# Performance work log

Hardware: AMD Instinct MI355X
Metric: run time of the kernel (lower is better)

## Reference

```python
import jax, jax.numpy as jnp
import numpy as np
from jax import lax

B, CIN, H, W = 16, 64, 128, 128
NUM_CLASSES = 80
K = 100              # cfg.TEST.TOPK
SCORE_THRESH = 0.2   # hardcoded in decode()
NMS_THRESH = 0.5     # cfg.TEST.NMS_THRESH
RATIO = 4.0          # inp_downsample_ratio


def setup_inputs() -> dict:
    key = jax.random.key(0)
    ks = jax.random.split(key, 8)
    def w(k, shape, scale=0.05):
        return jax.random.normal(k, shape, dtype=jnp.float32) * scale
    inp = {"x": jax.random.normal(ks[0], (B, CIN, H, W), dtype=jnp.float32)}
    for i, (name, cout) in enumerate([("cls", NUM_CLASSES), ("reg", 2), ("wh", 2)]):
        inp[f"{name}_w1"] = w(ks[1 + 2 * i], (64, CIN, 3, 3))
        inp[f"{name}_b1"] = jnp.zeros((64,), jnp.float32)
        inp[f"{name}_w2"] = w(ks[2 + 2 * i], (cout, 64, 1, 1))
        # cls 1x1 conv bias filled with -2.19 as in the torch module
        inp[f"{name}_b2"] = jnp.full((cout,), -2.19 if name == "cls" else 0.0, jnp.float32)
    return inp


def _conv(x, w, b):
    y = lax.conv_general_dilated(x, w, (1, 1), 'SAME',
                                 dimension_numbers=('NCHW', 'OIHW', 'NCHW'))
    return y + b[None, :, None, None]


def _branch(x, w1, b1, w2, b2):
    return _conv(jax.nn.relu(_conv(x, w1, b1)), w2, b2)


def _nms_keep(boxes, valid):
    # boxes: [K,4] sorted by score desc (top_k output); valid: [K] bool
    x1, y1, x2, y2 = boxes[:, 0], boxes[:, 1], boxes[:, 2], boxes[:, 3]
    area = (x2 - x1) * (y2 - y1)
    iw = jnp.clip(jnp.minimum(x2[:, None], x2[None, :]) - jnp.maximum(x1[:, None], x1[None, :]), 0.0)
    ih = jnp.clip(jnp.minimum(y2[:, None], y2[None, :]) - jnp.maximum(y1[:, None], y1[None, :]), 0.0)
    inter = iw * ih
    iou = inter / (area[:, None] + area[None, :] - inter + 1e-9)  # [K,K]
    idx = jnp.arange(K)
    def step(keep, i):
        sup = (iou[i] > NMS_THRESH) & (idx > i) & keep[i]
        return keep & ~sup, None
    keep, _ = lax.scan(step, valid, idx)
    return keep


def reference(x, cls_w1, cls_b1, cls_w2, cls_b2,
              reg_w1, reg_b1, reg_w2, reg_b2,
              wh_w1, wh_b1, wh_w2, wh_b2):
    cls = jax.nn.sigmoid(_branch(x, cls_w1, cls_b1, cls_w2, cls_b2))  # [B,C,H,W]
    reg = jax.nn.sigmoid(_branch(x, reg_w1, reg_b1, reg_w2, reg_b2))  # [B,2,H,W]
    wh = jnp.exp(_branch(x, wh_w1, wh_b1, wh_w2, wh_b2))              # [B,2,H,W]

    # 3x3 max-pool peak NMS (torch max_pool2d pads with -inf; SAME matches k=3,s=1,p=1)
    pooled = lax.reduce_window(cls, -jnp.inf, lax.max, (1, 1, 3, 3), (1, 1, 1, 1), 'SAME')
    cls = cls * (pooled == cls).astype(cls.dtype)

    cls_f = cls.transpose(0, 2, 3, 1).reshape(B, H * W, NUM_CLASSES)
    reg_f = reg.transpose(0, 2, 3, 1).reshape(B, H * W, 2)
    wh_f = wh.transpose(0, 2, 3, 1).reshape(B, H * W, 2)

    scores_all = jnp.max(cls_f, axis=-1)              # [B,HW]
    cats_all = jnp.argmax(cls_f, axis=-1)             # [B,HW]
    scores, inds = lax.top_k(scores_all, K)           # [B,K], sorted desc
    valid = scores > SCORE_THRESH                     # fixed-size mask instead of dynamic filter

    cats = jnp.take_along_axis(cats_all, inds, axis=1)
    reg_k = jnp.take_along_axis(reg_f, inds[..., None], axis=1)   # [B,K,2]
    wh_k = jnp.take_along_axis(wh_f, inds[..., None], axis=1)     # [B,K,2]

    gy, gx = jnp.meshgrid(jnp.arange(H), jnp.arange(W), indexing='ij')
    grids = jnp.stack([gx, gy], axis=-1).reshape(-1, 2).astype(jnp.float32)  # [HW,2] (x,y)
    ct = grids[inds] + reg_k                                       # [B,K,2]
    boxes = jnp.concatenate([ct - wh_k / 2.0, ct + wh_k / 2.0], axis=-1) * RATIO  # [B,K,4]

    keep = jax.vmap(_nms_keep)(boxes, valid)          # [B,K] bool
    return boxes, cats, scores, keep
```

## Files before the change

### kernel.cpp

```cpp
#include <hip/hip_runtime.h>
#include <math.h>

#define BN 16
#define HWSZ 16384
#define NC 80
#define KK 100

typedef _Float16 f16;
typedef _Float16 f16x2 __attribute__((ext_vector_type(2)));
typedef _Float16 f16x4 __attribute__((ext_vector_type(4)));
typedef _Float16 f16x8 __attribute__((ext_vector_type(8)));
typedef float    f32x4 __attribute__((ext_vector_type(4)));
typedef unsigned int uint;
typedef unsigned long long u64;

#define WS_CLS   0
#define CLS_SZ   (BN*NC*HWSZ)
#define WS_REG   (WS_CLS + CLS_SZ)
#define REG_SZ   (BN*2*HWSZ)
#define WS_WH    (WS_REG + REG_SZ)
#define WH_SZ    (BN*2*HWSZ)
#define WS_SC    (WS_WH + WH_SZ)
#define SC_SZ    (BN*HWSZ)
#define WS_CAT   (WS_SC + SC_SZ)
#define CAT_SZ   (BN*HWSZ)
#define WS_W1H   (WS_CAT + CAT_SZ)
#define W1F      (110592/2)
#define WS_W1L   (WS_W1H + W1F)
#define WS_W2H   (WS_W1L + W1F)
#define W2F      (7168/2)
#define WS_W2L   (WS_W2H + W2F)
#define NREG     (BN*128*2*2)
#define WS_XTH   (WS_W2L + W2F)
#define XT_F     (NREG*2112/2)
#define WS_XTL   (WS_XTH + XT_F)
#define WS_ZR    (WS_XTL + XT_F)
#define ZR_F     1056
#define WS_SC1   (WS_ZR + ZR_F)
#define WS_CAT1  (WS_SC1 + SC_SZ)
#define WS_END2  (WS_CAT1 + CAT_SZ)

#define SCL_X   16.0f
#define SCL_W   256.0f
#define INV_ACC (1.0f/4096.0f)

#define GL2LDS(g, l) __builtin_amdgcn_global_load_lds( \
    (__attribute__((address_space(1))) unsigned int*)(unsigned long long)(const void*)(g), \
    (__attribute__((address_space(3))) unsigned int*)(unsigned int)(unsigned long long)(void*)(l), \
    16, 0, 0)

__global__ void k_prep(const float* __restrict__ cw1, const float* __restrict__ rw1,
                       const float* __restrict__ ww1, const float* __restrict__ cw2,
                       const float* __restrict__ rw2, const float* __restrict__ ww2,
                       f16* __restrict__ w1h, f16* __restrict__ w1l,
                       f16* __restrict__ w2h, f16* __restrict__ w2l,
                       float* __restrict__ zr) {
    int idx = blockIdx.x * 256 + threadIdx.x;
    if (idx < 3*9*64*64) {
        int ci = idx & 63, co = (idx >> 6) & 63;
        int s  = (idx >> 12) % 9, br = idx / 36864;
        const float* src = (br == 0) ? cw1 : (br == 1 ? rw1 : ww1);
        float v = src[(co*64 + ci)*9 + s] * SCL_W;
        f16 h = (f16)v;
        w1h[idx] = h; w1l[idx] = (f16)(v - (float)h);
    }
    int j = idx - 3*9*64*64;
    if (j >= 0 && j < 112*64) {
        int ci = j & 63, row = j >> 6;
        float v = 0.f;
        if (row < 80)                    v = cw2[row*64 + ci];
        else if (row < 82)               v = rw2[(row-80)*64 + ci];
        else if (row >= 96 && row < 98)  v = ww2[(row-96)*64 + ci];
        v *= SCL_W;
        f16 h = (f16)v;
        w2h[j] = h; w2l[j] = (f16)(v - (float)h);
    }
    if (zr && idx < ZR_F) zr[idx] = 0.f;
}

__global__ __launch_bounds__(256) void k_prepx(const float* __restrict__ x,
                                               f16* __restrict__ xth,
                                               f16* __restrict__ xtl) {
    const int reg = blockIdx.x;
    const int chunk = reg & 1, hh = (reg >> 1) & 1;
    const int gy = (reg >> 2) & 127, b = reg >> 9;
    __shared__ f16 th[66*72] __attribute__((aligned(16)));
    __shared__ f16 tl[66*72] __attribute__((aligned(16)));
    const int tid = threadIdx.x;
    const float* xb = x + ((size_t)(b*64 + chunk*32))*HWSZ + gy*128;
    #pragma unroll
    for (int it = 0; it < 9; it++) {
        int idx = it*256 + tid;
        if (idx < 2112) {
            int ci = idx / 66, pxi = idx - ci*66;
            int gp = hh*64 - 1 + pxi;
            float v = 0.f;
            if (gp >= 0 && gp < 128) v = xb[(size_t)ci*HWSZ + gp] * SCL_X;
            f16 hv = (f16)v;
            th[pxi*72 + ci] = hv;
            tl[pxi*72 + ci] = (f16)(v - (float)hv);
        }
    }
    __syncthreads();
    f16* oh = xth + (size_t)reg*2112;
    f16* ol = xtl + (size_t)reg*2112;
    {
        int row = tid >> 2, q = tid & 3;
        int sq = q ^ ((row >> 1) & 3);
        *(f16x8*)(oh + row*32 + sq*8) = *(const f16x8*)(th + row*72 + q*8);
        *(f16x8*)(ol + row*32 + sq*8) = *(const f16x8*)(tl + row*72 + q*8);
        if (tid < 8) {
            int u2 = 256 + tid, row2 = u2 >> 2, q2 = u2 & 3;
            int sq2 = q2 ^ ((row2 >> 1) & 3);
            *(f16x8*)(oh + row2*32 + sq2*8) = *(const f16x8*)(th + row2*72 + q2*8);
            *(f16x8*)(ol + row2*32 + sq2*8) = *(const f16x8*)(tl + row2*72 + q2*8);
        }
    }
}

#define ABUF 8448
__global__ __launch_bounds__(256) void k_conv(
    const f16* __restrict__ xth, const f16* __restrict__ xtl, const f16* __restrict__ zreg,
    const f16* __restrict__ w1h, const f16* __restrict__ w1l,
    const f16* __restrict__ w2h, const f16* __restrict__ w2l,
    const float* __restrict__ b1c, const float* __restrict__ b1r, const float* __restrict__ b1w,
    const float* __restrict__ b2c, const float* __restrict__ b2r, const float* __restrict__ b2w,
    float* __restrict__ cls_o, float* __restrict__ reg_o, float* __restrict__ wh_o)
{
    __shared__ char smem[6*ABUF] __attribute__((aligned(16)));
    f16* Rh = (f16*)smem;
    f16* Rl = (f16*)(smem + 9216);

    const int p  = blockIdx.x + 2*blockIdx.y + 256*blockIdx.z;
    const int lg = (p & 7)*512 + (p >> 3);
    const int b  = lg >> 8;
    const int y  = (lg & 255) >> 1;
    const int h  = lg & 1;

    const int tid = threadIdx.x;
    const int w = tid >> 6, lane = tid & 63;
    const int l15 = lane & 15, quad = lane >> 4;

    static const int CS[6] = {0,0,0,1,1,1};
    static const int RS[6] = {0,1,2,0,1,2};

    #pragma unroll
    for (int si = 0; si < 6; si++) {
        const int gy_ = y - 1 + RS[si];
        const f16* sh_; const f16* sl_;
        if (gy_ >= 0 && gy_ < 128) {
            size_t ro_ = (size_t)(((b*128 + gy_)*2 + h)*2 + CS[si]) * 2112;
            sh_ = xth + ro_; sl_ = xtl + ro_;
        } else { sh_ = zreg; sl_ = zreg; }
        char* db_ = smem + si*ABUF;
        GL2LDS(sh_ + tid*8, db_ + tid*16);
        GL2LDS(sl_ + tid*8, db_ + 4224 + tid*16);
        if (tid < 8) {
            GL2LDS(sh_ + 2048 + tid*8, db_ + 4096 + tid*16);
            GL2LDS(sl_ + 2048 + tid*8, db_ + 4224 + 4096 + tid*16);
        }
    }

    f32x4 acc[3][4];
    #pragma unroll
    for (int br = 0; br < 3; br++)
        #pragma unroll
        for (int m = 0; m < 4; m++) acc[br][m] = (f32x4){0.f,0.f,0.f,0.f};

    __syncthreads();

    for (int si = 0; si < 6; si++) {
        const f16* APh = (const f16*)(smem + si*ABUF);
        const f16* APl = APh + 2112;
        const int chunk = CS[si], r = RS[si];
        #pragma unroll
        for (int dx = 0; dx < 3; dx++) {
            const int s = r*3 + dx;
            f16x8 bh[3], bl[3];
            #pragma unroll
            for (int br = 0; br < 3; br++) {
                size_t k = ((size_t)((br*9 + s)*64 + (w*16 + l15)))*64 + chunk*32 + quad*8;
                bh[br] = *(const f16x8*)(w1h + k);
                bl[br] = *(const f16x8*)(w1l + k);
            }
            #pragma unroll
            for (int m = 0; m < 4; m++) {
                const int row = m*16 + l15 + dx;
                const int off = row*32 + ((quad ^ ((row >> 1) & 3)) << 3);
                f16x8 ah = *(const f16x8*)(APh + off);
                f16x8 al = *(const f16x8*)(APl + off);
                #pragma unroll
                for (int br = 0; br < 3; br++) {
                    acc[br][m] = __builtin_amdgcn_mfma_f32_16x16x32_f16(ah, bh[br], acc[br][m], 0,0,0);
                    acc[br][m] = __builtin_amdgcn_mfma_f32_16x16x32_f16(ah, bl[br], acc[br][m], 0,0,0);
                    acc[br][m] = __builtin_amdgcn_mfma_f32_16x16x32_f16(al, bh[br], acc[br][m], 0,0,0);
                }
            }
        }
    }

    #pragma unroll
    for (int br = 0; br < 3; br++) {
        const float* b1 = (br == 0) ? b1c : (br == 1 ? b1r : b1w);
        const float b1v = b1[w*16 + l15];
        __syncthreads();
        #pragma unroll
        for (int m = 0; m < 4; m++)
            #pragma unroll
            for (int rg = 0; rg < 4; rg++) {
                float t = fmaxf(acc[br][m][rg]*INV_ACC + b1v, 0.f) * SCL_X;
                f16 hh = (f16)t;
                int pxl = m*16 + quad*4 + rg;
                int co  = w*16 + l15;
                Rh[pxl*72 + co] = hh;
                Rl[pxl*72 + co] = (f16)(t - (float)hh);
            }
        __syncthreads();

        const int NT     = (br == 0) ? 5 : 1;
        const int rowoff = (br == 0) ? 0 : (br == 1 ? 80 : 96);
        f32x4 a2[5];
        #pragma unroll
        for (int n = 0; n < 5; n++) a2[n] = (f32x4){0.f,0.f,0.f,0.f};

        #pragma unroll
        for (int kc = 0; kc < 64; kc += 32) {
            int off = (w*16 + l15)*72 + kc + quad*8;
            f16x8 xh = *(const f16x8*)(Rh + off);
            f16x8 xl = *(const f16x8*)(Rl + off);
            #pragma unroll
            for (int n = 0; n < 5; n++) {
                if (n >= NT) break;
                const f16* g2h = w2h + (rowoff + n*16 + l15)*64 + kc + quad*8;
                const f16* g2l = w2l + (rowoff + n*16 + l15)*64 + kc + quad*8;
                f16x8 bh = *(const f16x8*)g2h;
                f16x8 bl = *(const f16x8*)g2l;
                a2[n] = __builtin_amdgcn_mfma_f32_16x16x32_f16(xh, bh, a2[n], 0,0,0);
                a2[n] = __builtin_amdgcn_mfma_f32_16x16x32_f16(xh, bl, a2[n], 0,0,0);
                a2[n] = __builtin_amdgcn_mfma_f32_16x16x32_f16(xl, bh, a2[n], 0,0,0);
            }
        }

        const int pxg = h*64 + w*16 + quad*4;
        if (br == 0) {
            #pragma unroll
            for (int n = 0; n < 5; n++) {
                int co2 = n*16 + l15;
                float bb = b2c[co2];
                #pragma unroll
                for (int rg = 0; rg < 4; rg++) {
                    float sv = a2[n][rg]*INV_ACC + bb;
                    cls_o[((size_t)(b*80 + co2)*128 + y)*128 + pxg + rg] = 1.f/(1.f + expf(-sv));
                }
            }
        } else {
            if (l15 < 2) {
                const float* b2 = (br == 1) ? b2r : b2w;
                float* outp     = (br == 1) ? reg_o : wh_o;
                float bb = b2[l15];
                #pragma unroll
                for (int rg = 0; rg < 4; rg++) {
                    float sv = a2[0][rg]*INV_ACC + bb;
                    float o  = (br == 1) ? (1.f/(1.f + expf(-sv))) : expf(sv);
                    outp[((size_t)(b*2 + l15))*HWSZ + y*128 + pxg + rg] = o;
                }
            }
        }
    }
}

#define A_STRIDE 36
#define ABUF_FB  9504
__global__ __launch_bounds__(256) void k_conv_fb(
    const float* __restrict__ x,
    const f16* __restrict__ w1h, const f16* __restrict__ w1l,
    const f16* __restrict__ w2h, const f16* __restrict__ w2l,
    const float* __restrict__ b1c, const float* __restrict__ b1r, const float* __restrict__ b1w,
    const float* __restrict__ b2c, const float* __restrict__ b2r, const float* __restrict__ b2w,
    float* __restrict__ cls_o, float* __restrict__ reg_o, float* __restrict__ wh_o)
{
    __shared__ char smem[19008] __attribute__((aligned(16)));
    f16* Rh = (f16*)smem;
    f16* Rl = (f16*)(smem + 9216);

    const int h = blockIdx.x, y = blockIdx.y, b = blockIdx.z;
    const int tid = threadIdx.x;
    const int w = tid >> 6, lane = tid & 63;
    const int l15 = lane & 15, quad = lane >> 4;

    static const int CS[6] = {0,0,0,1,1,1};
    static const int RS[6] = {0,1,2,0,1,2};

    #define STAGEF(bufi, si_) do {                                            \
        const int gy = y - 1 + RS[si_];                                       \
        const bool ok = (gy >= 0) && (gy < 128);                              \
        const float* xp = x + ((size_t)(b*64 + CS[si_]*32)*128 + gy)*128;     \
        f16x2* dh = (f16x2*)(smem + (bufi)*ABUF_FB);                          \
        f16x2* dl = (f16x2*)(smem + (bufi)*ABUF_FB + 4752);                   \
        _Pragma("unroll")                                                     \
        for (int e0 = 0; e0 < 1024; e0 += 256) {                              \
            int e = e0 + tid;                                                 \
            int pxl = e & 63, cp = e >> 6;                                    \
            float v0 = 0.f, v1 = 0.f;                                         \
            if (ok) { int g = h*64 + pxl;                                     \
                      v0 = xp[(size_t)(2*cp)*HWSZ + g]*SCL_X;                 \
                      v1 = xp[(size_t)(2*cp+1)*HWSZ + g]*SCL_X; }             \
            f16 h0 = (f16)v0, h1 = (f16)v1;                                   \
            f16 l0 = (f16)(v0 - (float)h0), l1 = (f16)(v1 - (float)h1);       \
            int wi = (pxl + 1)*18 + cp;                                       \
            dh[wi] = (f16x2){h0, h1};                                         \
            dl[wi] = (f16x2){l0, l1};                                         \
        }                                                                     \
        if (tid < 32) {                                                       \
            int side = tid >> 4, cp = tid & 15;                               \
            bool valid = ok && (side ? (h == 0) : (h == 1));                  \
            int g = side ? 64 : 63;                                           \
            float v0 = 0.f, v1 = 0.f;                                         \
            if (valid) { v0 = xp[(size_t)(2*cp)*HWSZ + g]*SCL_X;              \
                         v1 = xp[(size_t)(2*cp+1)*HWSZ + g]*SCL_X; }          \
            f16 h0 = (f16)v0, h1 = (f16)v1;                                   \
            f16 l0 = (f16)(v0 - (float)h0), l1 = (f16)(v1 - (float)h1);       \
            int wi = (side ? 65 : 0)*18 + cp;                                 \
            dh[wi] = (f16x2){h0, h1};                                         \
            dl[wi] = (f16x2){l0, l1};                                         \
        }                                                                     \
    } while (0)

    f32x4 acc[3][4];
    #pragma unroll
    for (int br = 0; br < 3; br++)
        #pragma unroll
        for (int m = 0; m < 4; m++) acc[br][m] = (f32x4){0.f,0.f,0.f,0.f};

    STAGEF(0, 0);
    __syncthreads();

    for (int si = 0; si < 6; si++) {
        const int cur = si & 1;
        if (si < 5) STAGEF(cur ^ 1, si + 1);
        const f16* APh = (const f16*)(smem + cur*ABUF_FB);
        const f16* APl = APh + 2376;
        const int chunk = CS[si], r = RS[si];
        #pragma unroll
        for (int dx = 0; dx < 3; dx++) {
            const int s = r*3 + dx;
            f16x8 bh[3], bl[3];
            #pragma unroll
            for (int br = 0; br < 3; br++) {
                size_t k = ((size_t)((br*9 + s)*64 + (w*16 + l15)))*64 + chunk*32 + quad*8;
                bh[br] = *(const f16x8*)(w1h + k);
                bl[br] = *(const f16x8*)(w1l + k);
            }
            #pragma unroll
            for (int m = 0; m < 4; m++) {
                int off = (m*16 + l15 + dx)*A_STRIDE + quad*8;
                f16x4 h0 = *(const f16x4*)(APh + off);
                f16x4 h1 = *(const f16x4*)(APh + off + 4);
                f16x4 u0 = *(const f16x4*)(APl + off);
                f16x4 u1 = *(const f16x4*)(APl + off + 4);
                f16x8 ah = __builtin_shufflevector(h0, h1, 0,1,2,3,4,5,6,7);
                f16x8 al = __builtin_shufflevector(u0, u1, 0,1,2,3,4,5,6,7);
                #pragma unroll
                for (int br = 0; br < 3; br++) {
                    acc[br][m] = __builtin_amdgcn_mfma_f32_16x16x32_f16(ah, bh[br], acc[br][m], 0,0,0);
                    acc[br][m] = __builtin_amdgcn_mfma_f32_16x16x32_f16(ah, bl[br], acc[br][m], 0,0,0);
                    acc[br][m] = __builtin_amdgcn_mfma_f32_16x16x32_f16(al, bh[br], acc[br][m], 0,0,0);
                }
            }
        }
        __syncthreads();
    }
    #undef STAGEF

    #pragma unroll
    for (int br = 0; br < 3; br++) {
        const float* b1 = (br == 0) ? b1c : (br == 1 ? b1r : b1w);
        const float b1v = b1[w*16 + l15];
        __syncthreads();
        #pragma unroll
        for (int m = 0; m < 4; m++)
            #pragma unroll
            for (int rg = 0; rg < 4; rg++) {
                float t = fmaxf(acc[br][m][rg]*INV_ACC + b1v, 0.f) * SCL_X;
                f16 hh = (f16)t;
                int pxl = m*16 + quad*4 + rg;
                int co  = w*16 + l15;
                Rh[pxl*72 + co] = hh;
                Rl[pxl*72 + co] = (f16)(t - (float)hh);
            }
        __syncthreads();

        const int NT     = (br == 0) ? 5 : 1;
        const int rowoff = (br == 0) ? 0 : (br == 1 ? 80 : 96);
        f32x4 a2[5];
        #pragma unroll
        for (int n = 0; n < 5; n++) a2[n] = (f32x4){0.f,0.f,0.f,0.f};

        #pragma unroll
        for (int kc = 0; kc < 64; kc += 32) {
            int off = (w*16 + l15)*72 + kc + quad*8;
            f16x8 xh = *(const f16x8*)(Rh + off);
            f16x8 xl = *(const f16x8*)(Rl + off);
            #pragma unroll
            for (int n = 0; n < 5; n++) {
                if (n >= NT) break;
                const f16* g2h = w2h + (rowoff + n*16 + l15)*64 + kc + quad*8;
                const f16* g2l = w2l + (rowoff + n*16 + l15)*64 + kc + quad*8;
                f16x8 bh = *(const f16x8*)g2h;
                f16x8 bl = *(const f16x8*)g2l;
                a2[n] = __builtin_amdgcn_mfma_f32_16x16x32_f16(xh, bh, a2[n], 0,0,0);
                a2[n] = __builtin_amdgcn_mfma_f32_16x16x32_f16(xh, bl, a2[n], 0,0,0);
                a2[n] = __builtin_amdgcn_mfma_f32_16x16x32_f16(xl, bh, a2[n], 0,0,0);
            }
        }

        const int pxg = h*64 + w*16 + quad*4;
        if (br == 0) {
            #pragma unroll
            for (int n = 0; n < 5; n++) {
                int co2 = n*16 + l15;
                float bb = b2c[co2];
                #pragma unroll
                for (int rg = 0; rg < 4; rg++) {
                    float sv = a2[n][rg]*INV_ACC + bb;
                    cls_o[((size_t)(b*80 + co2)*128 + y)*128 + pxg + rg] = 1.f/(1.f + expf(-sv));
                }
            }
        } else {
            if (l15 < 2) {
                const float* b2 = (br == 1) ? b2r : b2w;
                float* outp     = (br == 1) ? reg_o : wh_o;
                float bb = b2[l15];
                #pragma unroll
                for (int rg = 0; rg < 4; rg++) {
                    float sv = a2[0][rg]*INV_ACC + bb;
                    float o  = (br == 1) ? (1.f/(1.f + expf(-sv))) : expf(sv);
                    outp[((size_t)(b*2 + l15))*HWSZ + y*128 + pxg + rg] = o;
                }
            }
        }
    }
}

__global__ __launch_bounds__(256) void k_peaks(const float* __restrict__ cls,
                                               float* __restrict__ scA,
                                               int* __restrict__ catA,
                                               float* __restrict__ scB,
                                               int* __restrict__ catB,
                                               int span) {
    const int b  = blockIdx.y;
    const int z  = blockIdx.z;
    const int c0 = z * span, c1 = c0 + span;
    float* __restrict__ sc  = z ? scB  : scA;
    int*   __restrict__ cat = z ? catB : catA;
    const int wv = threadIdx.x >> 6;
    const int l  = threadIdx.x & 63;
    const int y  = blockIdx.x * 4 + wv;
    const int p0 = l * 2;
    const bool yt = (y > 0), yb = (y < 127);
    float best0 = -1.f, best1 = -1.f;
    int bc0 = c0, bc1 = c0;
    for (int c = c0; c < c1; c++) {
        const float* pl = cls + (size_t)(b*80 + c)*HWSZ + y*128 + p0;
        float2 cur = *(const float2*)pl;
        float2 tp  = yt ? *(const float2*)(pl - 128) : make_float2(-1e30f, -1e30f);
        float2 bt  = yb ? *(const float2*)(pl + 128) : make_float2(-1e30f, -1e30f);
        float vm0 = fmaxf(cur.x, fmaxf(tp.x, bt.x));
        float vm1 = fmaxf(cur.y, fmaxf(tp.y, bt.y));
        float lft = __shfl_up(vm1, 1);   if (l == 0)  lft = -1e30f;
        float rgt = __shfl_down(vm0, 1); if (l == 63) rgt = -1e30f;
        float m0 = fmaxf(lft, fmaxf(vm0, vm1));
        float m1 = fmaxf(vm0, fmaxf(vm1, rgt));
        float k0 = (cur.x == m0) ? cur.x : 0.f;
        float k1 = (cur.y == m1) ? cur.y : 0.f;
        if (k0 > best0) { best0 = k0; bc0 = c; }
        if (k1 > best1) { best1 = k1; bc1 = c; }
    }
    int o = b*HWSZ + y*128 + p0;
    *(float2*)&sc[o] = make_float2(best0, best1);
    *(int2*)&cat[o]  = make_int2(bc0, bc1);
}

__global__ __launch_bounds__(256) void k_merge(float* __restrict__ sc0,
                                               int* __restrict__ cat0,
                                               const float* __restrict__ sc1,
                                               const int* __restrict__ cat1) {
    int i = (blockIdx.x * 256 + threadIdx.x) * 4;
    float4 a = *(const float4*)(sc0 + i);
    float4 bq = *(const float4*)(sc1 + i);
    int4   ca = *(const int4*)(cat0 + i);
    int4   cb = *(const int4*)(cat1 + i);
    if (bq.x > a.x) { a.x = bq.x; ca.x = cb.x; }
    if (bq.y > a.y) { a.y = bq.y; ca.y = cb.y; }
    if (bq.z > a.z) { a.z = bq.z; ca.z = cb.z; }
    if (bq.w > a.w) { a.w = bq.w; ca.w = cb.w; }
    *(float4*)(sc0 + i) = a;
    *(int4*)(cat0 + i)  = ca;
}

__global__ __launch_bounds__(256) void k_select(const float* __restrict__ sc,
                                                const int* __restrict__ cats,
                                                const float* __restrict__ regp,
                                                const float* __restrict__ whp,
                                                float* __restrict__ out) {
    const int b   = blockIdx.x;
    const int tid = threadIdx.x;
    const int wv  = tid >> 6, lane = tid & 63;
    const float* scb = sc + (size_t)b*HWSZ;

    __shared__ int   red[2][4];
    __shared__ uint  wtot[4];
    __shared__ int   gib[128];
    __shared__ uint  gvb[128];
    __shared__ int   ebuf[KK];
    __shared__ u64   keys[128];
    __shared__ int   s_inds[KK];
    __shared__ float s_vals[KK];
    __shared__ float X1[KK], Y1[KK], X2[KK], Y2[KK], AR[KK];

    f32x4 d[16];
    #pragma unroll
    for (int c = 0; c < 16; c++)
        d[c] = *(const f32x4*)(scb + c*1024 + tid*4);

    #define CNT_GT(T, OUTV) do {                                              \
        int myc_ = 0;                                                         \
        _Pragma("unroll")                                                     \
        for (int c = 0; c < 16; c++) {                                        \
            _Pragma("unroll")                                                 \
            for (int j = 0; j < 4; j++)                                       \
                myc_ += (__float_as_uint(d[c][j]) > (T)) ? 1 : 0;             \
        }                                                                     \
        _Pragma("unroll")                                                     \
        for (int o_ = 32; o_ >= 1; o_ >>= 1) myc_ += __shfl_xor(myc_, o_);    \
        if (lane == 0) red[par][wv] = myc_;                                   \
        __syncthreads();                                                      \
        OUTV = red[par][0] + red[par][1] + red[par][2] + red[par][3];         \
        par ^= 1;                                                             \
    } while (0)

    int par = 0;
    uint Vbits; uint G;
    {
        int tot0; CNT_GT(0u, tot0);
        if (tot0 < KK) { Vbits = 0u; G = (uint)tot0; }
        else {
            uint lo = 0u, hi = 0x7F800000u; int gHi = 0;
            while (hi - lo > 1u) {
                uint mid = lo + ((hi - lo) >> 1);
                int t_; CNT_GT(mid, t_);
                if (t_ >= KK) lo = mid; else { hi = mid; gHi = t_; }
            }
            Vbits = hi; G = (uint)gHi;
        }
    }
    #undef CNT_GT
    const uint Eneed = KK - G;

    f32x4 c4[16];
    #pragma unroll
    for (int c = 0; c < 16; c++)
        c4[c] = *(const f32x4*)(scb + tid*64 + c*4);

    uint cntG = 0, cntE = 0;
    #pragma unroll
    for (int c = 0; c < 16; c++)
        #pragma unroll
        for (int j = 0; j < 4; j++) {
            uint u = __float_as_uint(c4[c][j]);
            cntG += (u > Vbits) ? 1u : 0u;
            cntE += (u == Vbits) ? 1u : 0u;
        }
    uint pk = (cntE << 16) | cntG;
    uint v = pk;
    #pragma unroll
    for (int o = 1; o <= 32; o <<= 1) {
        uint ov = __shfl_up(v, o);
        if (lane >= o) v += ov;
    }
    if (lane == 63) wtot[wv] = v;
    __syncthreads();
    uint woff = 0;
    for (int i = 0; i < 4; i++) if (i < wv) woff += wtot[i];
    uint excl = v - pk + woff;
    uint pG = excl & 0xFFFFu, pE = excl >> 16;

    #pragma unroll
    for (int c = 0; c < 16; c++)
        #pragma unroll
        for (int j = 0; j < 4; j++) {
            uint u = __float_as_uint(c4[c][j]);
            int idx = tid*64 + c*4 + j;
            if (u > Vbits) { gib[pG] = idx; gvb[pG] = u; pG++; }
            else if (u == Vbits) { if (pE < Eneed) ebuf[pE] = idx; pE++; }
        }
    __syncthreads();

    if (tid < 128)
        keys[tid] = (tid < (int)G) ? (((u64)(~gvb[tid]) << 32) | (uint)gib[tid])
                                   : ~0ull;
    for (uint k2 = 2; k2 <= 128; k2 <<= 1) {
        for (uint j = k2 >> 1; j > 0; j >>= 1) {
            __syncthreads();
            if (tid < 128) {
                uint i = (uint)tid, ixj = i ^ j;
                if (ixj > i) {
                    u64 a = keys[i], bb = keys[ixj];
                    bool up = ((i & k2) == 0);
                    if ((a > bb) == up) { keys[i] = bb; keys[ixj] = a; }
                }
            }
        }
    }
    __syncthreads();

    if (tid < KK) {
        if (tid < (int)G) {
            u64 kk2 = keys[tid];
            s_inds[tid] = (int)(uint)kk2;
            s_vals[tid] = __uint_as_float(~(uint)(kk2 >> 32));
        } else {
            s_inds[tid] = ebuf[tid - (int)G];
            s_vals[tid] = __uint_as_float(Vbits);
        }
    }
    __syncthreads();

    if (tid < KK) {
        int ind   = s_inds[tid];
        float scv = s_vals[tid];
        const float* rb = regp + (size_t)b*2*HWSZ;
        const float* wb = whp  + (size_t)b*2*HWSZ;
        float r0 = rb[ind], r1 = rb[HWSZ + ind];
        float w0 = wb[ind], w1 = wb[HWSZ + ind];
        float ctx = (float)(ind & 127) + r0;
        float cty = (float)(ind >> 7) + r1;
        float x1 = (ctx - w0*0.5f)*4.f, y1 = (cty - w1*0.5f)*4.f;
        float x2 = (ctx + w0*0.5f)*4.f, y2 = (cty + w1*0.5f)*4.f;
        size_t bo = ((size_t)b*KK + tid)*4;
        out[bo+0] = x1; out[bo+1] = y1; out[bo+2] = x2; out[bo+3] = y2;
        out[BN*KK*4 + b*KK + tid]         = (float)cats[(size_t)b*HWSZ + ind];
        out[BN*KK*4 + BN*KK + b*KK + tid] = scv;
        X1[tid] = x1; Y1[tid] = y1; X2[tid] = x2; Y2[tid] = y2;
        AR[tid] = (x2 - x1)*(y2 - y1);
    }
    __syncthreads();

    if (tid < 64) {
        const int l = tid;
        float x1a = X1[l], y1a = Y1[l], x2a = X2[l], y2a = Y2[l], ara = AR[l];
        int   ka  = (s_vals[l] > 0.2f) ? 1 : 0;
        float x1b = 0, y1b = 0, x2b = 0, y2b = 0, arb = 0;
        int   kb  = 0;
        if (l < KK - 64) {
            x1b = X1[64+l]; y1b = Y1[64+l]; x2b = X2[64+l]; y2b = Y2[64+l];
            arb = AR[64+l];
            kb  = (s_vals[64+l] > 0.2f) ? 1 : 0;
        }
        for (int i = 0; i < KK; i++) {
            float jx1, jy1, jx2, jy2, jar; int jk;
            if (i < 64) {
                jx1 = __shfl(x1a, i); jy1 = __shfl(y1a, i);
                jx2 = __shfl(x2a, i); jy2 = __shfl(y2a, i);
                jar = __shfl(ara, i); jk  = __shfl(ka,  i);
            } else {
                int li = i - 64;
                jx1 = __shfl(x1b, li); jy1 = __shfl(y1b, li);
                jx2 = __shfl(x2b, li); jy2 = __shfl(y2b, li);
                jar = __shfl(arb, li); jk  = __shfl(kb,  li);
            }
            if (jk) {
                if (ka && l > i) {
                    float iw = fminf(jx2, x2a) - fmaxf(jx1, x1a); iw = iw > 0.f ? iw : 0.f;
                    float ih = fminf(jy2, y2a) - fmaxf(jy1, y1a); ih = ih > 0.f ? ih : 0.f;
                    float inter = iw*ih;
                    float iou = inter / (jar + ara - inter + 1e-9f);
                    if (iou > 0.5f) ka = 0;
                }
                if (kb && (64 + l) > i) {
                    float iw = fminf(jx2, x2b) - fmaxf(jx1, x1b); iw = iw > 0.f ? iw : 0.f;
                    float ih = fminf(jy2, y2b) - fmaxf(jy1, y1b); ih = ih > 0.f ? ih : 0.f;
                    float inter = iw*ih;
                    float iou = inter / (jar + arb - inter + 1e-9f);
                    if (iou > 0.5f) kb = 0;
                }
            }
        }
        int koff = BN*KK*4 + 2*BN*KK;
        out[koff + b*KK + l] = ka ? 1.f : 0.f;
        if (l < KK - 64) out[koff + b*KK + 64 + l] = kb ? 1.f : 0.f;
    }
}

extern "C" void kernel_launch(void* const* d_in, const int* in_sizes, int n_in,
                              void* d_out, int out_size, void* d_ws, size_t ws_size,
                              hipStream_t stream) {
    const float* x      = (const float*)d_in[0];
    const float* cls_w1 = (const float*)d_in[1];
    const float* cls_b1 = (const float*)d_in[2];
    const float* cls_w2 = (const float*)d_in[3];
    const float* cls_b2 = (const float*)d_in[4];
    const float* reg_w1 = (const float*)d_in[5];
    const float* reg_b1 = (const float*)d_in[6];
    const float* reg_w2 = (const float*)d_in[7];
    const float* reg_b2 = (const float*)d_in[8];
    const float* wh_w1  = (const float*)d_in[9];
    const float* wh_b1  = (const float*)d_in[10];
    const float* wh_w2  = (const float*)d_in[11];
    const float* wh_b2  = (const float*)d_in[12];

    float* ws   = (float*)d_ws;
    float* clsb = ws + WS_CLS;
    float* regb = ws + WS_REG;
    float* whb  = ws + WS_WH;
    float* scw  = ws + WS_SC;
    int*   cat  = (int*)(ws + WS_CAT);
    f16*   w1h  = (f16*)(ws + WS_W1H);
    f16*   w1l  = (f16*)(ws + WS_W1L);
    f16*   w2h  = (f16*)(ws + WS_W2H);
    f16*   w2l  = (f16*)(ws + WS_W2L);
    f16*   xth  = (f16*)(ws + WS_XTH);
    f16*   xtl  = (f16*)(ws + WS_XTL);
    f16*   zr   = (f16*)(ws + WS_ZR);
    float* sc1  = ws + WS_SC1;
    int*   cat1 = (int*)(ws + WS_CAT1);
    float* out  = (float*)d_out;

    const bool big = ws_size >= (size_t)WS_END2 * 4u;

    k_prep<<<(3*9*64*64 + 112*64 + 255)/256, 256, 0, stream>>>(
        cls_w1, reg_w1, wh_w1, cls_w2, reg_w2, wh_w2, w1h, w1l, w2h, w2l,
        big ? (float*)(ws + WS_ZR) : (float*)0);
    if (big) {
        k_prepx<<<NREG, 256, 0, stream>>>(x, xth, xtl);
        k_conv<<<dim3(2, 128, 16), 256, 0, stream>>>(
            xth, xtl, zr, w1h, w1l, w2h, w2l, cls_b1, reg_b1, wh_b1,
            cls_b2, reg_b2, wh_b2, clsb, regb, whb);
        k_peaks<<<dim3(32, 16, 2), 256, 0, stream>>>(clsb, scw, cat, sc1, cat1, 40);
        k_merge<<<256, 256, 0, stream>>>(scw, cat, sc1, cat1);
    } else {
        k_conv_fb<<<dim3(2, 128, 16), 256, 0, stream>>>(
            x, w1h, w1l, w2h, w2l, cls_b1, reg_b1, wh_b1,
            cls_b2, reg_b2, wh_b2, clsb, regb, whb);
        k_peaks<<<dim3(32, 16, 1), 256, 0, stream>>>(clsb, scw, cat, scw, cat, 80);
    }
    k_select<<<16, 256, 0, stream>>>(scw, cat, regb, whb, out);
}
```

Baseline: 490.1 us.

## Compute two output rows per conv block and split peak search four ways

The 3x3 conv kernel now produces two adjacent output rows per block. It stages four input rows per channel chunk and reuses each weight fragment for two accumulator sets, which cuts the grid in half and lowers redundant input and weight loads. LDS drops from six row buffers to four, and launch bounds request two blocks per CU, but doubling the accumulators raises register pressure. Separately, the peak search is split across four class slices instead of two, with a four-way merge kernel, at the cost of a larger workspace requirement.

```diff
diff --git a/kernel.cpp b/kernel.cpp
--- a/kernel.cpp
+++ b/kernel.cpp
@@ -38,7 +38,11 @@
 #define ZR_F     1056
 #define WS_SC1   (WS_ZR + ZR_F)
 #define WS_CAT1  (WS_SC1 + SC_SZ)
-#define WS_END2  (WS_CAT1 + CAT_SZ)
+#define WS_SC2   (WS_CAT1 + CAT_SZ)
+#define WS_CAT2  (WS_SC2 + SC_SZ)
+#define WS_SC3   (WS_CAT2 + CAT_SZ)
+#define WS_CAT3  (WS_SC3 + SC_SZ)
+#define WS_END4  (WS_CAT3 + CAT_SZ)
 
 #define SCL_X   16.0f
 #define SCL_W   256.0f
@@ -119,7 +123,7 @@
 }
 
 #define ABUF 8448
-__global__ __launch_bounds__(256) void k_conv(
+__global__ __launch_bounds__(256, 2) void k_conv(
     const f16* __restrict__ xth, const f16* __restrict__ xtl, const f16* __restrict__ zreg,
     const f16* __restrict__ w1h, const f16* __restrict__ w1l,
     const f16* __restrict__ w2h, const f16* __restrict__ w2l,
@@ -127,146 +131,166 @@
     const float* __restrict__ b2c, const float* __restrict__ b2r, const float* __restrict__ b2w,
     float* __restrict__ cls_o, float* __restrict__ reg_o, float* __restrict__ wh_o)
 {
-    __shared__ char smem[6*ABUF] __attribute__((aligned(16)));
+    __shared__ char smem[4*ABUF] __attribute__((aligned(16)));
     f16* Rh = (f16*)smem;
     f16* Rl = (f16*)(smem + 9216);
 
-    const int p  = blockIdx.x + 2*blockIdx.y + 256*blockIdx.z;
-    const int lg = (p & 7)*512 + (p >> 3);
-    const int b  = lg >> 8;
-    const int y  = (lg & 255) >> 1;
+    const int p  = blockIdx.x + 2*blockIdx.y + 128*blockIdx.z;
+    const int lg = (p & 7)*256 + (p >> 3);
+    const int b  = lg >> 7;
+    const int y0 = ((lg & 127) >> 1) * 2;
     const int h  = lg & 1;
 
     const int tid = threadIdx.x;
     const int w = tid >> 6, lane = tid & 63;
     const int l15 = lane & 15, quad = lane >> 4;
-
-    static const int CS[6] = {0,0,0,1,1,1};
-    static const int RS[6] = {0,1,2,0,1,2};
-
-    #pragma unroll
-    for (int si = 0; si < 6; si++) {
-        const int gy_ = y - 1 + RS[si];
-        const f16* sh_; const f16* sl_;
-        if (gy_ >= 0 && gy_ < 128) {
-            size_t ro_ = (size_t)(((b*128 + gy_)*2 + h)*2 + CS[si]) * 2112;
-            sh_ = xth + ro_; sl_ = xtl + ro_;
-        } else { sh_ = zreg; sl_ = zreg; }
-        char* db_ = smem + si*ABUF;
-        GL2LDS(sh_ + tid*8, db_ + tid*16);
-        GL2LDS(sl_ + tid*8, db_ + 4224 + tid*16);
-        if (tid < 8) {
-            GL2LDS(sh_ + 2048 + tid*8, db_ + 4096 + tid*16);
-            GL2LDS(sl_ + 2048 + tid*8, db_ + 4224 + 4096 + tid*16);
-        }
-    }
-
-    f32x4 acc[3][4];
+    const int co = w*16 + l15;
+
+    #define STAGE4(ch) do {                                                   \
+        _Pragma("unroll")                                                     \
+        for (int gyi = 0; gyi < 4; gyi++) {                                   \
+            const int gy_ = y0 - 1 + gyi;                                     \
+            const f16* sh_; const f16* sl_;                                   \
+            if (gy_ >= 0 && gy_ < 128) {                                      \
+                size_t ro_ = (size_t)(((b*128 + gy_)*2 + h)*2 + (ch)) * 2112; \
+                sh_ = xth + ro_; sl_ = xtl + ro_;                             \
+            } else { sh_ = zreg; sl_ = zreg; }                                \
+            char* db_ = smem + gyi*ABUF;                                      \
+            GL2LDS(sh_ + tid*8, db_ + tid*16);                                \
+            GL2LDS(sl_ + tid*8, db_ + 4224 + tid*16);                         \
+            if (tid < 8) {                                                    \
+                GL2LDS(sh_ + 2048 + tid*8, db_ + 4096 + tid*16);              \
+                GL2LDS(sl_ + 2048 + tid*8, db_ + 4224 + 4096 + tid*16);       \
+            }                                                                 \
+        }                                                                     \
+    } while (0)
+
+    f32x4 accA[3][4], accB[3][4];
     #pragma unroll
     for (int br = 0; br < 3; br++)
         #pragma unroll
-        for (int m = 0; m < 4; m++) acc[br][m] = (f32x4){0.f,0.f,0.f,0.f};
-
-    __syncthreads();
-
-    for (int si = 0; si < 6; si++) {
-        const f16* APh = (const f16*)(smem + si*ABUF);
-        const f16* APl = APh + 2112;
-        const int chunk = CS[si], r = RS[si];
-        #pragma unroll
-        for (int dx = 0; dx < 3; dx++) {
-            const int s = r*3 + dx;
-            f16x8 bh[3], bl[3];
-            #pragma unroll
-            for (int br = 0; br < 3; br++) {
-                size_t k = ((size_t)((br*9 + s)*64 + (w*16 + l15)))*64 + chunk*32 + quad*8;
-                bh[br] = *(const f16x8*)(w1h + k);
-                bl[br] = *(const f16x8*)(w1l + k);
-            }
-            #pragma unroll
-            for (int m = 0; m < 4; m++) {
-                const int row = m*16 + l15 + dx;
-                const int off = row*32 + ((quad ^ ((row >> 1) & 3)) << 3);
-                f16x8 ah = *(const f16x8*)(APh + off);
-                f16x8 al = *(const f16x8*)(APl + off);
-                #pragma unroll
-                for (int br = 0; br < 3; br++) {
-                    acc[br][m] = __builtin_amdgcn_mfma_f32_16x16x32_f16(ah, bh[br], acc[br][m], 0,0,0);
-                    acc[br][m] = __builtin_amdgcn_mfma_f32_16x16x32_f16(ah, bl[br], acc[br][m], 0,0,0);
-                    acc[br][m] = __builtin_amdgcn_mfma_f32_16x16x32_f16(al, bh[br], acc[br][m], 0,0,0);
-                }
-            }
-        }
-    }
+        for (int m = 0; m < 4; m++) {
+            accA[br][m] = (f32x4){0.f,0.f,0.f,0.f};
+            accB[br][m] = (f32x4){0.f,0.f,0.f,0.f};
+        }
+
+    #define COMPUTE(ph) do {                                                  \
+        for (int r = 0; r < 3; r++) {                                         \
+            const f16* A0 = (const f16*)(smem + r*ABUF);                      \
+            const f16* A1 = (const f16*)(smem + (r+1)*ABUF);                  \
+            _Pragma("unroll")                                                 \
+            for (int dx = 0; dx < 3; dx++) {                                  \
+                const int s = r*3 + dx;                                       \
+                f16x8 bh[3], bl[3];                                           \
+                _Pragma("unroll")                                             \
+                for (int br = 0; br < 3; br++) {                              \
+                    size_t k = ((size_t)((br*9 + s)*64 + co))*64 + (ph)*32 + quad*8; \
+                    bh[br] = *(const f16x8*)(w1h + k);                        \
+                    bl[br] = *(const f16x8*)(w1l + k);                        \
+                }                                                             \
+                _Pragma("unroll")                                             \
+                for (int m = 0; m < 4; m++) {                                 \
+                    const int row = m*16 + l15 + dx;                          \
+                    const int off = row*32 + ((quad ^ ((row >> 1) & 3)) << 3);\
+                    f16x8 ah0 = *(const f16x8*)(A0 + off);                    \
+                    f16x8 al0 = *(const f16x8*)(A0 + 2112 + off);             \
+                    f16x8 ah1 = *(const f16x8*)(A1 + off);                    \
+                    f16x8 al1 = *(const f16x8*)(A1 + 2112 + off);             \
+                    _Pragma("unroll")                                         \
+                    for (int br = 0; br < 3; br++) {                          \
+                        accA[br][m] = __builtin_amdgcn_mfma_f32_16x16x32_f16(ah0, bh[br], accA[br][m], 0,0,0); \
+                        accA[br][m] = __builtin_amdgcn_mfma_f32_16x16x32_f16(ah0, bl[br], accA[br][m], 0,0,0); \
+                        accA[br][m] = __builtin_amdgcn_mfma_f32_16x16x32_f16(al0, bh[br], accA[br][m], 0,0,0); \
+                        accB[br][m] = __builtin_amdgcn_mfma_f32_16x16x32_f16(ah1, bh[br], accB[br][m], 0,0,0); \
+                        accB[br][m] = __builtin_amdgcn_mfma_f32_16x16x32_f16(ah1, bl[br], accB[br][m], 0,0,0); \
+                        accB[br][m] = __builtin_amdgcn_mfma_f32_16x16x32_f16(al1, bh[br], accB[br][m], 0,0,0); \
+                    }                                                         \
+                }                                                             \
+            }                                                                 \
+        }                                                                     \
+    } while (0)
+
+    STAGE4(0);
+    __syncthreads();
+    COMPUTE(0);
+    __syncthreads();
+    STAGE4(1);
+    __syncthreads();
+    COMPUTE(1);
+
+    #undef STAGE4
+    #undef COMPUTE
+
+    #define EPIROW(ACC, yy) do {                                              \
+        __syncthreads();                        \
+        _Pragma("unroll")                                                     \
+        for (int m = 0; m < 4; m++)                                           \
+            _Pragma("unroll")                                                 \
+            for (int rg = 0; rg < 4; rg++) {                                  \
+                float t = fmaxf(ACC[br][m][rg]*INV_ACC + b1v, 0.f) * SCL_X;   \
+                f16 hh = (f16)t;                                              \
+                int pxl = m*16 + quad*4 + rg;                                 \
+                Rh[pxl*72 + co] = hh;                                         \
+                Rl[pxl*72 + co] = (f16)(t - (float)hh);                       \
+            }                                                                 \
+        __syncthreads();                                                      \
+        const int NT     = (br == 0) ? 5 : 1;                                 \
+        const int rowoff = (br == 0) ? 0 : (br == 1 ? 80 : 96);               \
+        f32x4 a2[5];                                                          \
+        _Pragma("unroll")                                                     \
+        for (int n = 0; n < 5; n++) a2[n] = (f32x4){0.f,0.f,0.f,0.f};         \
+        _Pragma("unroll")                                                     \
+        for (int kc = 0; kc < 64; kc += 32) {                                 \
+            int off = co*72 + kc + quad*8;                                    \
+            f16x8 xh = *(const f16x8*)(Rh + off);                             \
+            f16x8 xl = *(const f16x8*)(Rl + off);                             \
+            _Pragma("unroll")                                                 \
+            for (int n = 0; n < 5; n++) {                                     \
+                if (n >= NT) break;                                           \
+                const f16* g2h = w2h + (rowoff + n*16 + l15)*64 + kc + quad*8;\
+                const f16* g2l = w2l + (rowoff + n*16 + l15)*64 + kc + quad*8;\
+                f16x8 bh2 = *(const f16x8*)g2h;                               \
+                f16x8 bl2 = *(const f16x8*)g2l;                               \
+                a2[n] = __builtin_amdgcn_mfma_f32_16x16x32_f16(xh, bh2, a2[n], 0,0,0); \
+                a2[n] = __builtin_amdgcn_mfma_f32_16x16x32_f16(xh, bl2, a2[n], 0,0,0); \
+                a2[n] = __builtin_amdgcn_mfma_f32_16x16x32_f16(xl, bh2, a2[n], 0,0,0); \
+            }                                                                 \
+        }                                                                     \
+        const int pxg = h*64 + w*16 + quad*4;                                 \
+        if (br == 0) {                                                        \
+            _Pragma("unroll")                                                 \
+            for (int n = 0; n < 5; n++) {                                     \
+                int co2 = n*16 + l15;                                         \
+                float bb = b2c[co2];                                          \
+                _Pragma("unroll")                                             \
+                for (int rg = 0; rg < 4; rg++) {                              \
+                    float sv = a2[n][rg]*INV_ACC + bb;                        \
+                    cls_o[((size_t)(b*80 + co2)*128 + (yy))*128 + pxg + rg] = 1.f/(1.f + expf(-sv)); \
+                }                                                             \
+            }                                                                 \
+        } else {                                                              \
+            if (l15 < 2) {                                                    \
+                const float* b2 = (br == 1) ? b2r : b2w;                      \
+                float* outp     = (br == 1) ? reg_o : wh_o;                   \
+                float bb = b2[l15];                                           \
+                _Pragma("unroll")                                             \
+                for (int rg = 0; rg < 4; rg++) {                              \
+                    float sv = a2[0][rg]*INV_ACC + bb;                        \
+                    float o  = (br == 1) ? (1.f/(1.f + expf(-sv))) : expf(sv);\
+                    outp[((size_t)(b*2 + l15))*HWSZ + (yy)*128 + pxg + rg] = o; \
+                }                                                             \
+            }                                                                 \
+        }                                                                     \
+    } while (0)
 
     #pragma unroll
     for (int br = 0; br < 3; br++) {
         const float* b1 = (br == 0) ? b1c : (br == 1 ? b1r : b1w);
-        const float b1v = b1[w*16 + l15];
-        __syncthreads();
-        #pragma unroll
-        for (int m = 0; m < 4; m++)
-            #pragma unroll
-            for (int rg = 0; rg < 4; rg++) {
-                float t = fmaxf(acc[br][m][rg]*INV_ACC + b1v, 0.f) * SCL_X;
-                f16 hh = (f16)t;
-                int pxl = m*16 + quad*4 + rg;
-                int co  = w*16 + l15;
-                Rh[pxl*72 + co] = hh;
-                Rl[pxl*72 + co] = (f16)(t - (float)hh);
-            }
-        __syncthreads();
-
-        const int NT     = (br == 0) ? 5 : 1;
-        const int rowoff = (br == 0) ? 0 : (br == 1 ? 80 : 96);
-        f32x4 a2[5];
-        #pragma unroll
-        for (int n = 0; n < 5; n++) a2[n] = (f32x4){0.f,0.f,0.f,0.f};
-
-        #pragma unroll
-        for (int kc = 0; kc < 64; kc += 32) {
-            int off = (w*16 + l15)*72 + kc + quad*8;
-            f16x8 xh = *(const f16x8*)(Rh + off);
-            f16x8 xl = *(const f16x8*)(Rl + off);
-            #pragma unroll
-            for (int n = 0; n < 5; n++) {
-                if (n >= NT) break;
-                const f16* g2h = w2h + (rowoff + n*16 + l15)*64 + kc + quad*8;
-                const f16* g2l = w2l + (rowoff + n*16 + l15)*64 + kc + quad*8;
-                f16x8 bh = *(const f16x8*)g2h;
-                f16x8 bl = *(const f16x8*)g2l;
-                a2[n] = __builtin_amdgcn_mfma_f32_16x16x32_f16(xh, bh, a2[n], 0,0,0);
-                a2[n] = __builtin_amdgcn_mfma_f32_16x16x32_f16(xh, bl, a2[n], 0,0,0);
-                a2[n] = __builtin_amdgcn_mfma_f32_16x16x32_f16(xl, bh, a2[n], 0,0,0);
-            }
-        }
-
-        const int pxg = h*64 + w*16 + quad*4;
-        if (br == 0) {
-            #pragma unroll
-            for (int n = 0; n < 5; n++) {
-                int co2 = n*16 + l15;
-                float bb = b2c[co2];
-                #pragma unroll
-                for (int rg = 0; rg < 4; rg++) {
-                    float sv = a2[n][rg]*INV_ACC + bb;
-                    cls_o[((size_t)(b*80 + co2)*128 + y)*128 + pxg + rg] = 1.f/(1.f + expf(-sv));
-                }
-            }
-        } else {
-            if (l15 < 2) {
-                const float* b2 = (br == 1) ? b2r : b2w;
-                float* outp     = (br == 1) ? reg_o : wh_o;
-                float bb = b2[l15];
-                #pragma unroll
-                for (int rg = 0; rg < 4; rg++) {
-                    float sv = a2[0][rg]*INV_ACC + bb;
-                    float o  = (br == 1) ? (1.f/(1.f + expf(-sv))) : expf(sv);
-                    outp[((size_t)(b*2 + l15))*HWSZ + y*128 + pxg + rg] = o;
-                }
-            }
-        }
-    }
+        const float b1v = b1[co];
+        EPIROW(accA, y0);
+        EPIROW(accB, y0 + 1);
+    }
+    #undef EPIROW
 }
 
 #define A_STRIDE 36
@@ -443,16 +467,16 @@
 }
 
 __global__ __launch_bounds__(256) void k_peaks(const float* __restrict__ cls,
-                                               float* __restrict__ scA,
-                                               int* __restrict__ catA,
-                                               float* __restrict__ scB,
-                                               int* __restrict__ catB,
+                                               float* __restrict__ scA, int* __restrict__ catA,
+                                               float* __restrict__ scB, int* __restrict__ catB,
+                                               float* __restrict__ scC, int* __restrict__ catC,
+                                               float* __restrict__ scD, int* __restrict__ catD,
                                                int span) {
     const int b  = blockIdx.y;
     const int z  = blockIdx.z;
     const int c0 = z * span, c1 = c0 + span;
-    float* __restrict__ sc  = z ? scB  : scA;
-    int*   __restrict__ cat = z ? catB : catA;
+    float* __restrict__ sc  = (z == 0) ? scA  : (z == 1) ? scB  : (z == 2) ? scC  : scD;
+    int*   __restrict__ cat = (z == 0) ? catA : (z == 1) ? catB : (z == 2) ? catC : catD;
     const int wv = threadIdx.x >> 6;
     const int l  = threadIdx.x & 63;
     const int y  = blockIdx.x * 4 + wv;
@@ -481,19 +505,37 @@
     *(int2*)&cat[o]  = make_int2(bc0, bc1);
 }
 
-__global__ __launch_bounds__(256) void k_merge(float* __restrict__ sc0,
-                                               int* __restrict__ cat0,
-                                               const float* __restrict__ sc1,
-                                               const int* __restrict__ cat1) {
+__global__ __launch_bounds__(256) void k_merge4(float* __restrict__ sc0, int* __restrict__ cat0,
+                                                const float* __restrict__ s1, const int* __restrict__ c1,
+                                                const float* __restrict__ s2, const int* __restrict__ c2,
+                                                const float* __restrict__ s3, const int* __restrict__ c3) {
     int i = (blockIdx.x * 256 + threadIdx.x) * 4;
     float4 a = *(const float4*)(sc0 + i);
-    float4 bq = *(const float4*)(sc1 + i);
     int4   ca = *(const int4*)(cat0 + i);
-    int4   cb = *(const int4*)(cat1 + i);
-    if (bq.x > a.x) { a.x = bq.x; ca.x = cb.x; }
-    if (bq.y > a.y) { a.y = bq.y; ca.y = cb.y; }
-    if (bq.z > a.z) { a.z = bq.z; ca.z = cb.z; }
-    if (bq.w > a.w) { a.w = bq.w; ca.w = cb.w; }
+    {
+        float4 bq = *(const float4*)(s1 + i);
+        int4   cb = *(const int4*)(c1 + i);
+        if (bq.x > a.x) { a.x = bq.x; ca.x = cb.x; }
+        if (bq.y > a.y) { a.y = bq.y; ca.y = cb.y; }
+        if (bq.z > a.z) { a.z = bq.z; ca.z = cb.z; }
+        if (bq.w > a.w) { a.w = bq.w; ca.w = cb.w; }
+    }
+    {
+        float4 bq = *(const float4*)(s2 + i);
+        int4   cb = *(const int4*)(c2 + i);
+        if (bq.x > a.x) { a.x = bq.x; ca.x = cb.x; }
+        if (bq.y > a.y) { a.y = bq.y; ca.y = cb.y; }
+        if (bq.z > a.z) { a.z = bq.z; ca.z = cb.z; }
+        if (bq.w > a.w) { a.w = bq.w; ca.w = cb.w; }
+    }
+    {
+        float4 bq = *(const float4*)(s3 + i);
+        int4   cb = *(const int4*)(c3 + i);
+        if (bq.x > a.x) { a.x = bq.x; ca.x = cb.x; }
+        if (bq.y > a.y) { a.y = bq.y; ca.y = cb.y; }
+        if (bq.z > a.z) { a.z = bq.z; ca.z = cb.z; }
+        if (bq.w > a.w) { a.w = bq.w; ca.w = cb.w; }
+    }
     *(float4*)(sc0 + i) = a;
     *(int4*)(cat0 + i)  = ca;
 }
@@ -724,25 +766,31 @@
     f16*   zr   = (f16*)(ws + WS_ZR);
     float* sc1  = ws + WS_SC1;
     int*   cat1 = (int*)(ws + WS_CAT1);
+    float* sc2  = ws + WS_SC2;
+    int*   cat2 = (int*)(ws + WS_CAT2);
+    float* sc3  = ws + WS_SC3;
+    int*   cat3 = (int*)(ws + WS_CAT3);
     float* out  = (float*)d_out;
 
-    const bool big = ws_size >= (size_t)WS_END2 * 4u;
+    const bool big = ws_size >= (size_t)WS_END4 * 4u;
 
     k_prep<<<(3*9*64*64 + 112*64 + 255)/256, 256, 0, stream>>>(
         cls_w1, reg_w1, wh_w1, cls_w2, reg_w2, wh_w2, w1h, w1l, w2h, w2l,
         big ? (float*)(ws + WS_ZR) : (float*)0);
     if (big) {
         k_prepx<<<NREG, 256, 0, stream>>>(x, xth, xtl);
-        k_conv<<<dim3(2, 128, 16), 256, 0, stream>>>(
+        k_conv<<<dim3(2, 64, 16), 256, 0, stream>>>(
             xth, xtl, zr, w1h, w1l, w2h, w2l, cls_b1, reg_b1, wh_b1,
             cls_b2, reg_b2, wh_b2, clsb, regb, whb);
-        k_peaks<<<dim3(32, 16, 2), 256, 0, stream>>>(clsb, scw, cat, sc1, cat1, 40);
-        k_merge<<<256, 256, 0, stream>>>(scw, cat, sc1, cat1);
+        k_peaks<<<dim3(32, 16, 4), 256, 0, stream>>>(
+            clsb, scw, cat, sc1, cat1, sc2, cat2, sc3, cat3, 20);
+        k_merge4<<<256, 256, 0, stream>>>(scw, cat, sc1, cat1, sc2, cat2, sc3, cat3);
     } else {
         k_conv_fb<<<dim3(2, 128, 16), 256, 0, stream>>>(
             x, w1h, w1l, w2h, w2l, cls_b1, reg_b1, wh_b1,
             cls_b2, reg_b2, wh_b2, clsb, regb, whb);
-        k_peaks<<<dim3(32, 16, 1), 256, 0, stream>>>(clsb, scw, cat, scw, cat, 80);
+        k_peaks<<<dim3(32, 16, 1), 256, 0, stream>>>(
+            clsb, scw, cat, scw, cat, scw, cat, scw, cat, 80);
     }
     k_select<<<16, 256, 0, stream>>>(scw, cat, regb, whb, out);
 }
```

Measured after the change: 453.7 us. 7.4% less time.
